# Kernel tuning notes

Hardware: AMD Instinct MI355X
Metric: run time of the kernel (lower is better)

The kernel has to match this reference:

```python
import jax, jax.numpy as jnp
import numpy as np

DEG = np.pi / 180.0
H_FOV = (-180.0 * DEG, 180.0 * DEG)   # azimuth fov (rad)
V_FOV = (-3.0 * DEG, 25.0 * DEG)      # elevation fov (rad), phi = -asin(z/r)
W = 2048  # int((h_fov[1]-h_fov[0]) / h_res), h_res = 360/2048 deg
H = 64    # int((v_fov[1]-v_fov[0]) / v_res), v_res = 28/64 deg
B = 8
N = 2_000_000


def setup_inputs() -> dict:
    key = jax.random.key(0)
    k1, k2, k3 = jax.random.split(key, 3)
    # realistic lidar-scale coordinates: wide xy spread, shallow z
    xyz = jax.random.normal(k1, (N, 3), jnp.float32) * jnp.array([30.0, 30.0, 3.0], jnp.float32)
    inten = jax.random.uniform(k2, (N, 1), dtype=jnp.float32)
    bs = jax.random.randint(k3, (N, 1), 0, B).astype(jnp.float32)  # batch idx stored as float col 0
    points = jnp.concatenate([bs, xyz, inten], axis=1)  # [N, 5]
    return {"points": points, "batch_size": B}


def reference(points, batch_size):
    # points: [N, 1+4] = (batch_idx, x, y, z, intensity)
    bs_idx = points[:, 0].astype(jnp.int32)
    xyz = points[:, 1:4]
    extra = points[:, 4:]

    # spherical projection: r, theta (azimuth, cw from +x), phi (elevation, cw from xy-plane)
    r = jnp.linalg.norm(xyz, axis=1, keepdims=True)                      # [N,1]
    theta = -jnp.arctan2(xyz[:, 1], xyz[:, 0])[:, None]                  # [N,1]
    phi = -jnp.arcsin(xyz[:, 2:3] / jnp.maximum(r, 1e-5))                # [N,1]

    u_n = (theta - H_FOV[0]) / (H_FOV[1] - H_FOV[0])                     # [N,1] normed col
    v_n = (phi - V_FOV[0]) / (V_FOV[1] - V_FOV[0])                       # [N,1] normed row

    mask = (u_n[:, 0] >= 0) & (u_n[:, 0] < 1) & (v_n[:, 0] >= 0) & (v_n[:, 0] < 1)

    u = (u_n[:, 0] * W).astype(jnp.int32)
    v = (v_n[:, 0] * H).astype(jnp.int32)
    # route masked-out points to an out-of-bounds index; scatter mode='drop' discards them
    u = jnp.where(mask, u, W)
    v = jnp.where(mask, v, H)

    # use_xyz=True: features = [xyz, rThetaPhi, raw_features] -> channels = 7
    features = jnp.concatenate([xyz, r, theta, phi, extra], axis=1)      # [N,7]

    rv = jnp.zeros((batch_size, H, W, features.shape[1]), points.dtype)
    rv = rv.at[bs_idx, v, u].set(features, mode='drop')
    return jnp.transpose(rv, (0, 3, 1, 2))  # [B, 7, H, W]
```

## Files before the change

kernel.cpp:

```cpp
#include <hip/hip_runtime.h>
#include <math.h>

#define W_IMG 2048
#define H_IMG 64
#define B_IMG 8
#define C_IMG 7
#define NPIX (B_IMG * H_IMG * W_IMG)

__device__ __forceinline__ float F(unsigned u) { return __uint_as_float(u); }
#define FMAF(a,b,c) __builtin_fmaf((a),(b),(c))

__device__ __forceinline__ float glibc_atanf(float x) {
    const float atanhi[4] = {F(0x3eed6338u), F(0x3f490fdau), F(0x3f7b985eu), F(0x3fc90fdau)};
    const float atanlo[4] = {F(0x31ac3769u), F(0x33222168u), F(0x33140fb4u), F(0x33a22168u)};
    const float aT0 = F(0x3eaaaaabu), aT1 = F(0xbe4ccccdu), aT2 = F(0x3e124925u),
                aT3 = F(0xbde38e38u), aT4 = F(0x3dba2e6eu), aT5 = F(0xbd9d8795u),
                aT6 = F(0x3d886b35u), aT7 = F(0xbd6ef16bu), aT8 = F(0x3d4bda59u),
                aT9 = F(0xbd15a221u), aT10 = F(0x3c8569d7u);

    unsigned hx = __float_as_uint(x);
    unsigned ix = hx & 0x7fffffffu;
    if (ix >= 0x4c800000u) {
        if (ix > 0x7f800000u) return x + x;
        float v = __fadd_rn(atanhi[3], atanlo[3]);
        return (hx >> 31) ? -v : v;
    }
    int id;
    float xr = x;
    if (ix < 0x3ee00000u) {
        if (ix < 0x31000000u) return x;
        id = -1;
    } else {
        xr = fabsf(x);
        if (ix < 0x3f980000u) {
            if (ix < 0x3f300000u) {
                id = 0;
                xr = __fdiv_rn(__fsub_rn(__fmul_rn(2.0f, xr), 1.0f),
                               __fadd_rn(2.0f, xr));
            } else {
                id = 1;
                xr = __fdiv_rn(__fsub_rn(xr, 1.0f), __fadd_rn(xr, 1.0f));
            }
        } else {
            if (ix < 0x401c0000u) {
                id = 2;
                xr = __fdiv_rn(__fsub_rn(xr, 1.5f),
                               __fadd_rn(1.0f, __fmul_rn(1.5f, xr)));
            } else {
                id = 3;
                xr = __fdiv_rn(-1.0f, xr);
            }
        }
    }
    float z = __fmul_rn(xr, xr);
    float w = __fmul_rn(z, z);
    float s1 = __fmul_rn(z, __fadd_rn(aT0, __fmul_rn(w, __fadd_rn(aT2,
               __fmul_rn(w, __fadd_rn(aT4, __fmul_rn(w, __fadd_rn(aT6,
               __fmul_rn(w, __fadd_rn(aT8, __fmul_rn(w, aT10)))))))))));
    float s2 = __fmul_rn(w, __fadd_rn(aT1, __fmul_rn(w, __fadd_rn(aT3,
               __fmul_rn(w, __fadd_rn(aT5, __fmul_rn(w, __fadd_rn(aT7,
               __fmul_rn(w, aT9)))))))));
    if (id < 0) return __fsub_rn(x, __fmul_rn(x, __fadd_rn(s1, s2)));
    const float hi[4] = {atanhi[0], atanhi[1], atanhi[2], atanhi[3]};
    const float lo[4] = {atanlo[0], atanlo[1], atanlo[2], atanlo[3]};
    float zz = __fsub_rn(hi[id],
               __fsub_rn(__fsub_rn(__fmul_rn(xr, __fadd_rn(s1, s2)), lo[id]), xr));
    return (hx >> 31) ? -zz : zz;
}

__device__ __forceinline__ float glibc_atan2f(float y, float x) {
    const float pi_o_2 = F(0x3fc90fdbu);
    const float pi     = F(0x40490fdbu);
    const float pi_lo  = F(0xb3bbbd2eu);
    unsigned hx = __float_as_uint(x), hy = __float_as_uint(y);
    unsigned ix = hx & 0x7fffffffu, iy = hy & 0x7fffffffu;
    if (ix > 0x7f800000u || iy > 0x7f800000u) return x + y;
    if (hx == 0x3f800000u) return glibc_atanf(y);
    unsigned m = ((hy >> 31) & 1u) | ((hx >> 30) & 2u);
    if (iy == 0) {
        switch (m) {
            case 0: case 1: return y;
            case 2: return pi;
            default: return -pi;
        }
    }
    if (ix == 0) return (m & 1u) ? -pi_o_2 : pi_o_2;
    if (ix == 0x7f800000u) {
        if (iy == 0x7f800000u) {
            switch (m) {
                case 0: return F(0x3f490fdbu);
                case 1: return -F(0x3f490fdbu);
                case 2: return __fmul_rn(3.0f, F(0x3f490fdbu));
                default: return -__fmul_rn(3.0f, F(0x3f490fdbu));
            }
        } else {
            switch (m) {
                case 0: return 0.0f;
                case 1: return -0.0f;
                case 2: return pi;
                default: return -pi;
            }
        }
    }
    if (iy == 0x7f800000u) return (m & 1u) ? -pi_o_2 : pi_o_2;

    int k = ((int)iy - (int)ix) >> 23;
    float z;
    if (k > 26) {
        z = __fadd_rn(pi_o_2, __fmul_rn(0.5f, pi_lo));
        m &= 1u;
    } else if (k < -26 && (hx >> 31)) {
        z = 0.0f;
    } else {
        z = glibc_atanf(fabsf(__fdiv_rn(y, x)));
    }
    switch (m) {
        case 0: return z;
        case 1: return __uint_as_float(__float_as_uint(z) ^ 0x80000000u);
        case 2: return __fsub_rn(pi, __fsub_rn(z, pi_lo));
        default: return __fsub_rn(__fsub_rn(z, pi_lo), pi);
    }
}

struct Proj {
    float r, theta, phi;
    int   pix;
    bool  in_image;
};

__device__ __forceinline__ Proj project_point(float x, float y, float z, float bsf) {
    const float H0F   = (float)(-3.14159265358979323846);
    const float SPANH = (float)( 6.28318530717958647692);
    const float V0F   = (float)(-3.0 * 3.14159265358979323846 / 180.0);
    const float SPANV = (float)((25.0 * 3.14159265358979323846 / 180.0) -
                                (-3.0 * 3.14159265358979323846 / 180.0));
    const float RH = 1.0f / SPANH;
    const float RV = 1.0f / SPANV;

    Proj p;
    p.r = __fsqrt_rn(FMAF(z, z, FMAF(y, y, __fmul_rn(x, x))));
    p.theta = -glibc_atan2f(y, x);

    float zr = __fdiv_rn(z, fmaxf(p.r, 1e-5f));
    float s  = __fsqrt_rn(FMAF(-zr, zr, 1.0f));
    float d  = __fadd_rn(1.0f, s);
    p.phi = -__fmul_rn(2.0f, glibc_atan2f(zr, d));

    float u_n = __fmul_rn(__fsub_rn(p.theta, H0F), RH);
    float v_n = __fmul_rn(__fsub_rn(p.phi,   V0F), RV);
    p.in_image = (u_n >= 0.0f) && (u_n < 1.0f) && (v_n >= 0.0f) && (v_n < 1.0f);
    p.pix = -1;
    if (p.in_image) {
        int u = (int)__fmul_rn(u_n, (float)W_IMG);
        int v = (int)__fmul_rn(v_n, (float)H_IMG);
        int b = (int)bsf;
        if (u < W_IMG && v < H_IMG) {
            p.pix = (b * H_IMG + v) * W_IMG + u;
        } else {
            p.in_image = false;
        }
    }
    return p;
}

__global__ void init_winner(int4* winner4, int n4) {
    int i = blockIdx.x * blockDim.x + threadIdx.x;
    if (i < n4) winner4[i] = make_int4(-1, -1, -1, -1);
}

__global__ void scatter_winner(const float* __restrict__ pts, int* __restrict__ winner, int n) {
    int i = blockIdx.x * blockDim.x + threadIdx.x;
    if (i >= n) return;
    const float* q = pts + (size_t)i * 5;
    Proj p = project_point(q[1], q[2], q[3], q[0]);
    if (p.in_image) {
        atomicMax(&winner[p.pix], i);
    }
}

__global__ void write_output(const float* __restrict__ pts, const int* __restrict__ winner,
                             float* __restrict__ out) {
    int p = blockIdx.x * blockDim.x + threadIdx.x;
    if (p >= NPIX) return;
    int wi = winner[p];
    int b  = p / (H_IMG * W_IMG);
    int hw = p - b * (H_IMG * W_IMG);

    float feat[C_IMG] = {0.f, 0.f, 0.f, 0.f, 0.f, 0.f, 0.f};
    if (wi >= 0) {
        const float* q = pts + (size_t)wi * 5;
        Proj pr = project_point(q[1], q[2], q[3], q[0]);
        feat[0] = q[1]; feat[1] = q[2]; feat[2] = q[3];
        feat[3] = pr.r; feat[4] = pr.theta; feat[5] = pr.phi;
        feat[6] = q[4];
    }
    size_t base = (size_t)b * C_IMG * H_IMG * W_IMG + hw;
#pragma unroll
    for (int c = 0; c < C_IMG; ++c) {
        out[base + (size_t)c * H_IMG * W_IMG] = feat[c];
    }
}

extern "C" void kernel_launch(void* const* d_in, const int* in_sizes, int n_in,
                              void* d_out, int out_size, void* d_ws, size_t ws_size,
                              hipStream_t stream) {
    const float* pts = (const float*)d_in[0];
    int n = in_sizes[0] / 5;
    int* winner = (int*)d_ws;
    float* out = (float*)d_out;

    int n4 = NPIX / 4;
    init_winner<<<(n4 + 255) / 256, 256, 0, stream>>>((int4*)winner, n4);
    scatter_winner<<<(n + 255) / 256, 256, 0, stream>>>(pts, winner, n);
    write_output<<<(NPIX + 255) / 256, 256, 0, stream>>>(pts, winner, out);
}
```

Measured before the change: 154.8 us.

## Vectorize point loads and output stores, early-reject out-of-FOV points

The scatter kernel now handles four points per thread, loading their 20 floats as five float4 reads. Before computing the costly atan2, it rejects any point whose z/r lies outside the elevation window. The write kernel handles four pixels per thread, with one int4 read of winner indices and float4 stores per channel. The atan table lookup now indexes the constant arrays directly instead of going through local copies. The early-reject thresholds are hand-picked constants, so points right at the elevation edges carry a small correctness risk, and fewer threads run per kernel.

```diff
diff --git a/kernel.cpp b/kernel.cpp
--- a/kernel.cpp
+++ b/kernel.cpp
@@ -5,7 +5,8 @@
 #define H_IMG 64
 #define B_IMG 8
 #define C_IMG 7
-#define NPIX (B_IMG * H_IMG * W_IMG)
+#define HW_IMG (H_IMG * W_IMG)
+#define NPIX (B_IMG * HW_IMG)
 
 __device__ __forceinline__ float F(unsigned u) { return __uint_as_float(u); }
 #define FMAF(a,b,c) __builtin_fmaf((a),(b),(c))
@@ -61,10 +62,8 @@
                __fmul_rn(w, __fadd_rn(aT5, __fmul_rn(w, __fadd_rn(aT7,
                __fmul_rn(w, aT9)))))))));
     if (id < 0) return __fsub_rn(x, __fmul_rn(x, __fadd_rn(s1, s2)));
-    const float hi[4] = {atanhi[0], atanhi[1], atanhi[2], atanhi[3]};
-    const float lo[4] = {atanlo[0], atanlo[1], atanlo[2], atanlo[3]};
-    float zz = __fsub_rn(hi[id],
-               __fsub_rn(__fsub_rn(__fmul_rn(xr, __fadd_rn(s1, s2)), lo[id]), xr));
+    float zz = __fsub_rn(atanhi[id],
+               __fsub_rn(__fsub_rn(__fmul_rn(xr, __fadd_rn(s1, s2)), atanlo[id]), xr));
     return (hx >> 31) ? -zz : zz;
 }
 
@@ -123,12 +122,12 @@
 }
 
 struct Proj {
-    float r, theta, phi;
+    float theta, phi;
     int   pix;
     bool  in_image;
 };
 
-__device__ __forceinline__ Proj project_point(float x, float y, float z, float bsf) {
+__device__ __forceinline__ Proj project_from(float x, float y, float zr, float bsf) {
     const float H0F   = (float)(-3.14159265358979323846);
     const float SPANH = (float)( 6.28318530717958647692);
     const float V0F   = (float)(-3.0 * 3.14159265358979323846 / 180.0);
@@ -138,10 +137,7 @@
     const float RV = 1.0f / SPANV;
 
     Proj p;
-    p.r = __fsqrt_rn(FMAF(z, z, FMAF(y, y, __fmul_rn(x, x))));
     p.theta = -glibc_atan2f(y, x);
-
-    float zr = __fdiv_rn(z, fmaxf(p.r, 1e-5f));
     float s  = __fsqrt_rn(FMAF(-zr, zr, 1.0f));
     float d  = __fadd_rn(1.0f, s);
     p.phi = -__fmul_rn(2.0f, glibc_atan2f(zr, d));
@@ -163,41 +159,96 @@
     return p;
 }
 
+__device__ __forceinline__ float norm_r(float x, float y, float z) {
+    return __fsqrt_rn(FMAF(z, z, FMAF(y, y, __fmul_rn(x, x))));
+}
+
 __global__ void init_winner(int4* winner4, int n4) {
     int i = blockIdx.x * blockDim.x + threadIdx.x;
     if (i < n4) winner4[i] = make_int4(-1, -1, -1, -1);
 }
 
 __global__ void scatter_winner(const float* __restrict__ pts, int* __restrict__ winner, int n) {
-    int i = blockIdx.x * blockDim.x + threadIdx.x;
-    if (i >= n) return;
-    const float* q = pts + (size_t)i * 5;
-    Proj p = project_point(q[1], q[2], q[3], q[0]);
-    if (p.in_image) {
-        atomicMax(&winner[p.pix], i);
+    int t  = blockIdx.x * blockDim.x + threadIdx.x;
+    int i0 = t * 4;
+    if (i0 >= n) return;
+
+    float bx[4], px[4], py[4], pz[4];
+    if (i0 + 4 <= n) {
+        const float4* p4 = (const float4*)(pts + (size_t)i0 * 5);
+        float4 c0 = p4[0], c1 = p4[1], c2 = p4[2], c3 = p4[3], c4 = p4[4];
+        bx[0] = c0.x; px[0] = c0.y; py[0] = c0.z; pz[0] = c0.w;
+        bx[1] = c1.y; px[1] = c1.z; py[1] = c1.w; pz[1] = c2.x;
+        bx[2] = c2.z; px[2] = c2.w; py[2] = c3.x; pz[2] = c3.y;
+        bx[3] = c3.w; px[3] = c4.x; py[3] = c4.y; pz[3] = c4.z;
+    } else {
+        for (int k = 0; k < 4; ++k) {
+            int i = i0 + k;
+            if (i < n) {
+                const float* q = pts + (size_t)i * 5;
+                bx[k] = q[0]; px[k] = q[1]; py[k] = q[2]; pz[k] = q[3];
+            } else {
+                bx[k] = 0.f; px[k] = 0.f; py[k] = 0.f; pz[k] = 1e9f;
+            }
+        }
+    }
+#pragma unroll
+    for (int k = 0; k < 4; ++k) {
+        float x = px[k], y = py[k], z = pz[k];
+        float r  = norm_r(x, y, z);
+        float zr = __fdiv_rn(z, fmaxf(r, 1e-5f));
+        if (zr > 0.05240f || zr < -0.42270f) continue;
+        Proj p = project_from(x, y, zr, bx[k]);
+        if (p.in_image) {
+            atomicMax(&winner[p.pix], i0 + k);
+        }
     }
 }
 
 __global__ void write_output(const float* __restrict__ pts, const int* __restrict__ winner,
                              float* __restrict__ out) {
-    int p = blockIdx.x * blockDim.x + threadIdx.x;
-    if (p >= NPIX) return;
-    int wi = winner[p];
-    int b  = p / (H_IMG * W_IMG);
-    int hw = p - b * (H_IMG * W_IMG);
-
-    float feat[C_IMG] = {0.f, 0.f, 0.f, 0.f, 0.f, 0.f, 0.f};
-    if (wi >= 0) {
-        const float* q = pts + (size_t)wi * 5;
-        Proj pr = project_point(q[1], q[2], q[3], q[0]);
-        feat[0] = q[1]; feat[1] = q[2]; feat[2] = q[3];
-        feat[3] = pr.r; feat[4] = pr.theta; feat[5] = pr.phi;
-        feat[6] = q[4];
-    }
-    size_t base = (size_t)b * C_IMG * H_IMG * W_IMG + hw;
+    int t  = blockIdx.x * blockDim.x + threadIdx.x;
+    int p0 = t * 4;
+    if (p0 >= NPIX) return;
+
+    int4 w4 = *(const int4*)(winner + p0);
+    int wis[4] = {w4.x, w4.y, w4.z, w4.w};
+
+    float qb[4], qx[4], qy[4], qz[4], qi[4];
+#pragma unroll
+    for (int k = 0; k < 4; ++k) {
+        if (wis[k] >= 0) {
+            const float* q = pts + (size_t)wis[k] * 5;
+            qb[k] = q[0]; qx[k] = q[1]; qy[k] = q[2]; qz[k] = q[3]; qi[k] = q[4];
+        }
+    }
+
+    float fc[C_IMG][4];
+#pragma unroll
+    for (int c = 0; c < C_IMG; ++c)
+#pragma unroll
+        for (int k = 0; k < 4; ++k) fc[c][k] = 0.f;
+
+#pragma unroll
+    for (int k = 0; k < 4; ++k) {
+        if (wis[k] >= 0) {
+            float x = qx[k], y = qy[k], z = qz[k];
+            float r  = norm_r(x, y, z);
+            float zr = __fdiv_rn(z, fmaxf(r, 1e-5f));
+            Proj pr = project_from(x, y, zr, qb[k]);
+            fc[0][k] = x; fc[1][k] = y; fc[2][k] = z;
+            fc[3][k] = r; fc[4][k] = pr.theta; fc[5][k] = pr.phi;
+            fc[6][k] = qi[k];
+        }
+    }
+
+    int b  = p0 >> 17;
+    int hw = p0 & (HW_IMG - 1);
+    size_t base = (size_t)b * C_IMG * HW_IMG + hw;
 #pragma unroll
     for (int c = 0; c < C_IMG; ++c) {
-        out[base + (size_t)c * H_IMG * W_IMG] = feat[c];
+        float4 v = make_float4(fc[c][0], fc[c][1], fc[c][2], fc[c][3]);
+        *(float4*)(out + base + (size_t)c * HW_IMG) = v;
     }
 }
 
@@ -211,6 +262,10 @@
 
     int n4 = NPIX / 4;
     init_winner<<<(n4 + 255) / 256, 256, 0, stream>>>((int4*)winner, n4);
-    scatter_winner<<<(n + 255) / 256, 256, 0, stream>>>(pts, winner, n);
-    write_output<<<(NPIX + 255) / 256, 256, 0, stream>>>(pts, winner, out);
-}
+
+    int nthreads = (n + 3) / 4;
+    scatter_winner<<<(nthreads + 255) / 256, 256, 0, stream>>>(pts, winner, n);
+
+    int pthreads = NPIX / 4;
+    write_output<<<(pthreads + 255) / 256, 256, 0, stream>>>(pts, winner, out);
+}
```

Result: no change. 157.8 us (+1.9%).
